# Kernel tuning notes

Hardware: AMD Instinct MI355X
Metric: run time of the kernel (lower is better)

Reference implementation:

```python
import jax, jax.numpy as jnp
import numpy as np

N_NODES, N_EDGES, NUM_GRAPHS = 50000, 800000, 64
F_DIM, H_DIM, N_LAYERS, N_CLASSES = 64, 64, 3, 16
EPS = 1e-5  # StdAggregation epsilon (PyG)


def setup_inputs() -> dict:
    key = jax.random.key(0)
    ks = jax.random.split(key, 12)
    s = 0.05
    x = jax.random.normal(ks[0], (N_NODES, F_DIM), jnp.float32)
    edge_index = jax.random.randint(ks[1], (2, N_EDGES), 0, N_NODES, dtype=jnp.int32)
    batch = jnp.sort(jax.random.randint(ks[2], (N_NODES,), 0, NUM_GRAPHS, dtype=jnp.int32))
    # per-layer PNAConv params (towers=1): pre Linear(2F->F), post Linear(13F->H), lin Linear(H->H)
    pre_w = jax.random.normal(ks[3], (N_LAYERS, F_DIM, 2 * F_DIM), jnp.float32) * s
    pre_b = jnp.zeros((N_LAYERS, F_DIM), jnp.float32)
    post_w = jax.random.normal(ks[4], (N_LAYERS, H_DIM, 13 * F_DIM), jnp.float32) * s
    post_b = jnp.zeros((N_LAYERS, H_DIM), jnp.float32)
    lin_w = jax.random.normal(ks[5], (N_LAYERS, H_DIM, H_DIM), jnp.float32) * s
    lin_b = jnp.zeros((N_LAYERS, H_DIM), jnp.float32)
    mlp_w1 = jax.random.normal(ks[6], (H_DIM, H_DIM), jnp.float32) * s
    mlp_b1 = jnp.zeros((H_DIM,), jnp.float32)
    mlp_w2 = jax.random.normal(ks[7], (N_CLASSES, H_DIM), jnp.float32) * s
    mlp_b2 = jnp.zeros((N_CLASSES,), jnp.float32)
    return dict(x=x, edge_index=edge_index, batch=batch,
                pre_w=pre_w, pre_b=pre_b, post_w=post_w, post_b=post_b,
                lin_w=lin_w, lin_b=lin_b, mlp_w1=mlp_w1, mlp_b1=mlp_b1,
                mlp_w2=mlp_w2, mlp_b2=mlp_b2)


def pna_forward(x, src, dst, pre_w, pre_b, post_w, post_b, lin_w, lin_b,
                mlp_w1, mlp_b1, mlp_w2, mlp_b2, batch):
    N = x.shape[0]
    deg_raw = jax.ops.segment_sum(jnp.ones_like(src, jnp.float32), dst, N)  # in-degree [N]
    deg = jnp.maximum(deg_raw, 1.0)[:, None]
    # avg log degree (PNA avg_deg['log'] from the degree histogram of this graph)
    avg_log = jnp.mean(jnp.log(deg_raw + 1.0))
    log_deg = jnp.log(deg + 1.0)
    amp = log_deg / avg_log          # amplification scaler [N,1]
    att = avg_log / log_deg          # attenuation scaler [N,1]
    has_in = (deg_raw > 0)[:, None]

    for l in range(pre_w.shape[0]):
        h = jnp.concatenate([x[dst], x[src]], axis=-1)        # [E, 2F] (x_i, x_j)
        m = h @ pre_w[l].T + pre_b[l]                          # pre_nn message [E, F]
        s1 = jax.ops.segment_sum(m, dst, N)
        s2 = jax.ops.segment_sum(m * m, dst, N)
        mean = s1 / deg
        std = jnp.sqrt(jax.nn.relu(s2 / deg - mean * mean) + EPS)
        mn = jnp.where(has_in, jax.ops.segment_min(m, dst, N), 0.0)
        mx = jnp.where(has_in, jax.ops.segment_max(m, dst, N), 0.0)
        aggr = jnp.concatenate([mean, mn, mx, std], axis=-1)   # [N, 4F]
        out = jnp.concatenate([x, aggr, aggr * amp, aggr * att], axis=-1)  # [N, 13F]
        out = out @ post_w[l].T + post_b[l]                    # post_nn [N, H]
        x = jax.nn.relu(out @ lin_w[l].T + lin_b[l])           # conv.lin + outer ReLU

    # global mean pool over graphs
    counts = jnp.maximum(
        jax.ops.segment_sum(jnp.ones((N,), x.dtype), batch, NUM_GRAPHS), 1.0)
    g = jax.ops.segment_sum(x, batch, NUM_GRAPHS) / counts[:, None]  # [G, H]
    g = jax.nn.relu(g @ mlp_w1.T + mlp_b1)
    return g @ mlp_w2.T + mlp_b2                               # [G, C]


def reference(x, edge_index, batch, pre_w, pre_b, post_w, post_b,
              lin_w, lin_b, mlp_w1, mlp_b1, mlp_w2, mlp_b2):
    src, dst = edge_index[0], edge_index[1]
    return pna_forward(x, src, dst, pre_w, pre_b, post_w, post_b,
                       lin_w, lin_b, mlp_w1, mlp_b1, mlp_w2, mlp_b2, batch)
```

## Files before the change

kernel.cpp:

```cpp
#include <hip/hip_runtime.h>
#include <math.h>

#define N_NODES   50000
#define N_EDGES   800000
#define NUM_GRAPHS 64
#define FDIM      64
#define HDIM      64
#define NLAYERS   3
#define NCLASSES  16
#define EPS       1e-5f

#define SCAN_CHUNK 1024
#define NCHUNKS ((N_NODES + SCAN_CHUNK - 1) / SCAN_CHUNK)

typedef unsigned short u16;
typedef unsigned int   u32;
typedef __attribute__((ext_vector_type(8))) short short8;
typedef __attribute__((ext_vector_type(4))) float floatx4;

#define WKS_LAYER 159744
#define PRES_LAYER 24576
#define KPOST_LDS_BYTES 106496

__device__ inline void split1(float f, u16& h, u16& m, u16& l) {
    u32 b  = __float_as_uint(f);
    u32 hb = b & 0xFFFF0000u;
    float r = f - __uint_as_float(hb);
    u32 mb = __float_as_uint(r) & 0xFFFF0000u;
    float r2 = r - __uint_as_float(mb);
    u32 lb = __float_as_uint(r2) & 0xFFFF0000u;
    h = (u16)(hb >> 16); m = (u16)(mb >> 16); l = (u16)(lb >> 16);
}

__device__ inline void gl_lds16(const void* g, void* l) {
    __builtin_amdgcn_global_load_lds(
        (const __attribute__((address_space(1))) u32*)g,
        (__attribute__((address_space(3))) u32*)l, 16, 0, 0);
}

__global__ __launch_bounds__(256) void k_comb(const float* __restrict__ post_w,
                                              const float* __restrict__ lin_w,
                                              const float* __restrict__ pre_w,
                                              const float* __restrict__ post_b,
                                              const float* __restrict__ lin_b,
                                              u16* __restrict__ WkS,
                                              u16* __restrict__ PreS,
                                              float* __restrict__ bcv,
                                              int* __restrict__ cnt,
                                              float* __restrict__ logsum) {
    int b = blockIdx.x, t = threadIdx.x;
    int zi = b * 256 + t;
    if (zi < N_NODES) cnt[zi] = 0;
    if (zi == 0) *logsum = 0.f;

    if (b < 624) {
        int c  = t & 63;
        int kl = t >> 6;
        int l  = b / 208;
        int o  = (b % 208) * 4 + kl;
        const float* lw = lin_w + (size_t)l * 4096 + c * 64;
        const float* pw = post_w + (size_t)l * 53248 + o;
        float acc = 0.f;
        #pragma unroll 8
        for (int j = 0; j < 64; ++j)
            acc += lw[j] * pw[(size_t)j * 832];
        u16 h, m, lo;
        split1(acc, h, m, lo);

        int kn;
        if (o < 64) kn = o;
        else {
            int s  = (o - 64) >> 8;
            int mm = (o - 64) & 255;
            int j  = mm >> 5, r = mm & 31;
            kn = 64 + j * 96 + s * 32 + r;
        }
        int ch  = kn >> 5;
        int kin = kn & 31;
        int n16 = c & 15, nt = c >> 4;
        int swk = (((kin >> 3) + (n16 >> 1)) & 3) * 8 + (kin & 7);
        size_t base = (size_t)l * WKS_LAYER + (size_t)ch * 6144
                    + nt * 512 + n16 * 32 + swk;
        WkS[base]        = h;
        WkS[base + 2048] = m;
        WkS[base + 4096] = lo;
    } else if (b == 624) {
        if (t < 192) {
            int l = t >> 6, c = t & 63;
            float acc = lin_b[l * 64 + c];
            for (int j = 0; j < 64; ++j)
                acc += lin_w[(size_t)l * 4096 + c * 64 + j] * post_b[l * 64 + j];
            bcv[l * 64 + c] = acc;
        }
    } else {
        int i = (b - 625) * 256 + t;
        int l = i >> 13;
        int rem = i & 8191;
        int c128 = rem >> 6;
        int k = rem & 63;
        float v;
        if (c128 < 64) v = pre_w[(size_t)l * 8192 + c128 * 128 + k];
        else           v = pre_w[(size_t)l * 8192 + (c128 - 64) * 128 + 64 + k];
        u16 h, m, lo;
        split1(v, h, m, lo);
        int ch = k >> 5, kin = k & 31;
        int nt = c128 >> 4, n16 = c128 & 15;
        int swk = (((kin >> 3) + (n16 >> 1)) & 3) * 8 + (kin & 7);
        size_t base = (size_t)l * PRES_LAYER + (size_t)ch * 12288
                    + nt * 512 + n16 * 32 + swk;
        PreS[base]        = h;
        PreS[base + 4096] = m;
        PreS[base + 8192] = lo;
    }
}

__global__ void k_count(const int* __restrict__ dst, int* __restrict__ cnt,
                        int* __restrict__ rank) {
    int e = blockIdx.x * 256 + threadIdx.x;
    if (e < N_EDGES) rank[e] = atomicAdd(&cnt[dst[e]], 1);
}

__global__ void k_chunk_sums(const int* __restrict__ cnt, int* __restrict__ bsum,
                             float* __restrict__ logsum) {
    __shared__ int   ired[256];
    __shared__ float lred[256];
    int b = blockIdx.x, t = threadIdx.x;
    int base = b * SCAN_CHUNK;
    int s = 0; float ls = 0.f;
    for (int i = t; i < SCAN_CHUNK; i += 256) {
        int idx = base + i;
        if (idx < N_NODES) {
            int v = cnt[idx];
            s += v;
            ls += logf((float)v + 1.0f);
        }
    }
    ired[t] = s; lred[t] = ls;
    __syncthreads();
    for (int off = 128; off > 0; off >>= 1) {
        if (t < off) { ired[t] += ired[t + off]; lred[t] += lred[t + off]; }
        __syncthreads();
    }
    if (t == 0) { bsum[b] = ired[0]; atomicAdd(logsum, lred[0]); }
}

__global__ void k_scan_top(const int* __restrict__ bsum, int* __restrict__ boff,
                           int* __restrict__ row_start) {
    if (threadIdx.x == 0) {
        int acc = 0;
        for (int i = 0; i < NCHUNKS; ++i) { boff[i] = acc; acc += bsum[i]; }
        row_start[N_NODES] = acc;
    }
}

__global__ void k_scan_chunks(const int* __restrict__ cnt, const int* __restrict__ boff,
                              int* __restrict__ row_start) {
    __shared__ int tsum[256];
    int b = blockIdx.x, t = threadIdx.x;
    int base = b * SCAN_CHUNK + t * 4;
    int v[4]; int s = 0;
    #pragma unroll
    for (int i = 0; i < 4; ++i) {
        int idx = base + i;
        v[i] = (idx < N_NODES) ? cnt[idx] : 0;
        s += v[i];
    }
    tsum[t] = s;
    __syncthreads();
    for (int off = 1; off < 256; off <<= 1) {
        int val = (t >= off) ? tsum[t - off] : 0;
        __syncthreads();
        tsum[t] += val;
        __syncthreads();
    }
    int excl = boff[b] + tsum[t] - s;
    #pragma unroll
    for (int i = 0; i < 4; ++i) {
        int idx = base + i;
        if (idx < N_NODES) row_start[idx] = excl;
        excl += v[i];
    }
}

__global__ void k_scatter(const int* __restrict__ src, const int* __restrict__ dst,
                          const int* __restrict__ rank,
                          const int* __restrict__ row_start,
                          int* __restrict__ csr_src) {
    int e = blockIdx.x * 256 + threadIdx.x;
    if (e < N_EDGES) {
        int d = dst[e];
        csr_src[row_start[d] + rank[e]] = src[e];
    }
}

__global__ void k_scal(const int* __restrict__ cnt, const float* __restrict__ logsum,
                       float* __restrict__ inv_deg, float* __restrict__ ampv,
                       float* __restrict__ attv, float* __restrict__ g_sum,
                       int* __restrict__ g_cnt) {
    int n = blockIdx.x * 256 + threadIdx.x;
    if (blockIdx.x == 0) {
        for (int i = threadIdx.x; i < 4096; i += 256) g_sum[i] = 0.f;
        if (threadIdx.x < 64) g_cnt[threadIdx.x] = 0;
    }
    if (n < N_NODES) {
        float avg = logsum[0] / (float)N_NODES;
        float degf = fmaxf((float)cnt[n], 1.0f);
        inv_deg[n] = 1.0f / degf;
        float ld = logf(degf + 1.0f);
        ampv[n] = ld / avg;
        attv[n] = avg / ld;
    }
}

__global__ __launch_bounds__(256, 4) void k_pre(const float* __restrict__ x,
                                                const u16* __restrict__ PreS,
                                                const float* __restrict__ pre_b,
                                                float* __restrict__ p,
                                                float* __restrict__ q) {
    __shared__ u16 ldsB[2 * 8192];
    int t = threadIdx.x;
    int w = t >> 6;
    int lane = t & 63;
    int m = lane & 15;
    int qh = lane >> 4;
    int rowBase = blockIdx.x * 64;

    int myrow = rowBase + 16 * w + m;
    bool vr = myrow < N_NODES;
    int crow = vr ? myrow : 0;
    const float* xrow = x + (size_t)crow * 64;

    int bo = m * 32 + ((qh + (m >> 1)) & 3) * 8;

    for (int u = w; u < 32; u += 4) {
        int ch = u >> 4, sp = (u >> 3) & 1, nt = u & 7;
        const char* g = (const char*)PreS + (size_t)ch * 24576 + sp * 8192
                      + nt * 1024 + lane * 16;
        char* l = (char*)ldsB + u * 1024;
        gl_lds16(g, l);
    }
    float fa[2][8];
    #pragma unroll
    for (int ch = 0; ch < 2; ++ch) {
        const float* sp = xrow + ch * 32 + qh * 8;
        float4 u0 = *(const float4*)sp;
        float4 u1 = *(const float4*)(sp + 4);
        fa[ch][0] = vr ? u0.x : 0.f; fa[ch][1] = vr ? u0.y : 0.f;
        fa[ch][2] = vr ? u0.z : 0.f; fa[ch][3] = vr ? u0.w : 0.f;
        fa[ch][4] = vr ? u1.x : 0.f; fa[ch][5] = vr ? u1.y : 0.f;
        fa[ch][6] = vr ? u1.z : 0.f; fa[ch][7] = vr ? u1.w : 0.f;
    }
    asm volatile("s_waitcnt vmcnt(0)" ::: "memory");
    __syncthreads();

    floatx4 acc[8] = {};
    #pragma unroll
    for (int ch = 0; ch < 2; ++ch) {
        union { u32 u[4]; short8 s8; } AH, AM;
        #pragma unroll
        for (int i = 0; i < 4; ++i) {
            float f0 = fa[ch][2 * i], f1 = fa[ch][2 * i + 1];
            u32 b0 = __float_as_uint(f0), b1 = __float_as_uint(f1);
            u32 h0 = b0 & 0xFFFF0000u,  h1 = b1 & 0xFFFF0000u;
            float r0 = f0 - __uint_as_float(h0);
            float r1 = f1 - __uint_as_float(h1);
            u32 m0 = __float_as_uint(r0) & 0xFFFF0000u;
            u32 m1 = __float_as_uint(r1) & 0xFFFF0000u;
            AH.u[i] = (h0 >> 16) | h1;
            AM.u[i] = (m0 >> 16) | m1;
        }
        const u16* Bb = ldsB + ch * 8192;
        #pragma unroll
        for (int nt = 0; nt < 8; ++nt) {
            short8 bH = *(const short8*)(Bb + nt * 512 + bo);
            short8 bM = *(const short8*)(Bb + 4096 + nt * 512 + bo);
            acc[nt] = __builtin_amdgcn_mfma_f32_16x16x32_bf16(AH.s8, bH, acc[nt], 0, 0, 0);
            acc[nt] = __builtin_amdgcn_mfma_f32_16x16x32_bf16(AH.s8, bM, acc[nt], 0, 0, 0);
            acc[nt] = __builtin_amdgcn_mfma_f32_16x16x32_bf16(AM.s8, bH, acc[nt], 0, 0, 0);
        }
    }

    int col = m;
    #pragma unroll
    for (int nt = 0; nt < 8; ++nt) {
        int cbase = (nt & 3) * 16 + col;
        float bias = (nt < 4) ? pre_b[cbase] : 0.f;
        float* outp = (nt < 4) ? p : q;
        #pragma unroll
        for (int reg = 0; reg < 4; ++reg) {
            int grow = rowBase + 16 * w + qh * 4 + reg;
            if (grow < N_NODES)
                outp[(size_t)grow * 64 + cbase] = acc[nt][reg] + bias;
        }
    }
}

__global__ __launch_bounds__(256) void k_aggr(const float* __restrict__ p,
                                              const float* __restrict__ q,
                                              const int* __restrict__ row_start,
                                              const int* __restrict__ csr_src,
                                              const float* __restrict__ inv_deg,
                                              float* __restrict__ aggr) {
    int wid  = (blockIdx.x * 256 + threadIdx.x) >> 6;
    int lane = threadIdx.x & 63;
    if (wid >= N_NODES) return;
    int n = wid;
    int beg = row_start[n], end = row_start[n + 1];
    float sum = 0.f, sq = 0.f;
    float mn = INFINITY, mx = -INFINITY;
    int e = beg;
    for (; e + 7 < end; e += 8) {
        float qv[8];
        #pragma unroll
        for (int u = 0; u < 8; ++u) {
            int s = csr_src[e + u];
            qv[u] = q[(size_t)s * 64 + lane];
        }
        #pragma unroll
        for (int u = 0; u < 8; ++u) {
            float m = qv[u];
            sum += m; sq += m * m;
            mn = fminf(mn, m); mx = fmaxf(mx, m);
        }
    }
    for (; e + 3 < end; e += 4) {
        float qv[4];
        #pragma unroll
        for (int u = 0; u < 4; ++u) {
            int s = csr_src[e + u];
            qv[u] = q[(size_t)s * 64 + lane];
        }
        #pragma unroll
        for (int u = 0; u < 4; ++u) {
            float m = qv[u];
            sum += m; sq += m * m;
            mn = fminf(mn, m); mx = fmaxf(mx, m);
        }
    }
    for (; e < end; ++e) {
        int s = csr_src[e];
        float m = q[(size_t)s * 64 + lane];
        sum += m; sq += m * m;
        mn = fminf(mn, m); mx = fmaxf(mx, m);
    }
    float* a = aggr + (size_t)n * 256;
    if (end <= beg) {
        a[lane]       = 0.f;
        a[64 + lane]  = 0.f;
        a[128 + lane] = 0.f;
        a[192 + lane] = sqrtf(EPS);
    } else {
        float pv = p[n * 64 + lane];
        float id = inv_deg[n];
        float meanq = sum * id;
        float var = fmaxf(sq * id - meanq * meanq, 0.f);
        a[lane]       = pv + meanq;
        a[64 + lane]  = pv + mn;
        a[128 + lane] = pv + mx;
        a[192 + lane] = sqrtf(var + EPS);
    }
}

__global__ __launch_bounds__(1024, 4) void k_post(const float* __restrict__ x,
                                                  const float* __restrict__ aggr,
                                                  const float* __restrict__ ampv,
                                                  const float* __restrict__ attv,
                                                  const u16* __restrict__ WkS,
                                                  const float* __restrict__ bc,
                                                  float* __restrict__ xout) {
    extern __shared__ u16 ldsB[];
    int t = threadIdx.x;
    int w = t >> 6;
    int lane = t & 63;
    int m = lane & 15;
    int qh = lane >> 4;
    int nh = blockIdx.x & 1;
    int rowBase = (blockIdx.x >> 1) * 512 + 32 * w;

    for (int u = w; u < 104; u += 16) {
        int ch = u >> 2;
        int sp = (u >> 1) & 1;
        int h2 = u & 1;
        const char* g = (const char*)WkS + ch * 12288 + sp * 4096
                      + nh * 2048 + h2 * 1024 + lane * 16;
        char* l = (char*)ldsB + u * 1024;
        gl_lds16(g, l);
    }

    int row0 = rowBase + m;
    int row1 = row0 + 16;
    int cr0 = (row0 < N_NODES) ? row0 : 0;
    int cr1 = (row1 < N_NODES) ? row1 : 0;
    const float* xr0 = x + (size_t)cr0 * 64;
    const float* xr1 = x + (size_t)cr1 * 64;
    const float* ar0 = aggr + (size_t)cr0 * 256;
    const float* ar1 = aggr + (size_t)cr1 * 256;

    int bo = m * 32 + ((qh + (m >> 1)) & 3) * 8;

    floatx4 accP0[2] = {}, accA0[2] = {}, accT0[2] = {};
    floatx4 accP1[2] = {}, accA1[2] = {}, accT1[2] = {};

    float f0[8], f1[8];
    union U8 { u32 u[4]; short8 s8; };
    U8 AH0, AM0, AH1, AM1;

    auto loadRaw = [&](const float* sp, float* f) {
        float4 u0 = *(const float4*)(sp + qh * 8);
        float4 u1 = *(const float4*)(sp + qh * 8 + 4);
        f[0] = u0.x; f[1] = u0.y; f[2] = u0.z; f[3] = u0.w;
        f[4] = u1.x; f[5] = u1.y; f[6] = u1.z; f[7] = u1.w;
    };
    auto split2 = [&](const float* f, U8& H, U8& M8) {
        #pragma unroll
        for (int i = 0; i < 4; ++i) {
            float v0 = f[2 * i], v1 = f[2 * i + 1];
            u32 b0 = __float_as_uint(v0), b1 = __float_as_uint(v1);
            u32 h0 = b0 & 0xFFFF0000u,  h1 = b1 & 0xFFFF0000u;
            float r0 = v0 - __uint_as_float(h0);
            float r1 = v1 - __uint_as_float(h1);
            u32 m0 = __float_as_uint(r0) & 0xFFFF0000u;
            u32 m1 = __float_as_uint(r1) & 0xFFFF0000u;
            H.u[i]  = (h0 >> 16) | h1;
            M8.u[i] = (m0 >> 16) | m1;
        }
    };
    #define MF(A, B, C) C = __builtin_amdgcn_mfma_f32_16x16x32_bf16((A).s8, (B), (C), 0, 0, 0)
    auto chunkMM = [&](int ch, floatx4* A0, floatx4* A1) {
        const u16* pB = ldsB + ch * 2048 + bo;
        short8 bH0 = *(const short8*)(pB);
        short8 bH1 = *(const short8*)(pB + 512);
        short8 bM0 = *(const short8*)(pB + 1024);
        short8 bM1 = *(const short8*)(pB + 1536);
        MF(AH0, bH0, A0[0]); MF(AH1, bH0, A1[0]); MF(AH0, bH1, A0[1]); MF(AH1, bH1, A1[1]);
        MF(AH0, bM0, A0[0]); MF(AH1, bM0, A1[0]); MF(AH0, bM1, A0[1]); MF(AH1, bM1, A1[1]);
        MF(AM0, bH0, A0[0]); MF(AM1, bH0, A1[0]); MF(AM0, bH1, A0[1]); MF(AM1, bH1, A1[1]);
    };

    loadRaw(xr0, f0); loadRaw(xr1, f1);
    asm volatile("s_waitcnt vmcnt(0)" ::: "memory");
    __syncthreads();

    split2(f0, AH0, AM0); split2(f1, AH1, AM1);
    loadRaw(xr0 + 32, f0); loadRaw(xr1 + 32, f1);
    chunkMM(0, accP0, accP1);
    split2(f0, AH0, AM0); split2(f1, AH1, AM1);
    loadRaw(ar0, f0); loadRaw(ar1, f1);
    chunkMM(1, accP0, accP1);
    for (int j = 0; j < 8; ++j) {
        split2(f0, AH0, AM0); split2(f1, AH1, AM1);
        if (j < 7) { loadRaw(ar0 + (j + 1) * 32, f0); loadRaw(ar1 + (j + 1) * 32, f1); }
        int ch = 2 + 3 * j;
        chunkMM(ch,     accP0, accP1);
        chunkMM(ch + 1, accA0, accA1);
        chunkMM(ch + 2, accT0, accT1);
    }
    #undef MF

    int col = m;
    #pragma unroll
    for (int frag = 0; frag < 2; ++frag) {
        #pragma unroll
        for (int reg = 0; reg < 4; ++reg) {
            int grow = rowBase + 16 * frag + qh * 4 + reg;
            if (grow < N_NODES) {
                float av = ampv[grow], tv = attv[grow];
                #pragma unroll
                for (int nt = 0; nt < 2; ++nt) {
                    int cbase = (nh * 2 + nt) * 16 + col;
                    float pv  = frag ? accP1[nt][reg] : accP0[nt][reg];
                    float av2 = frag ? accA1[nt][reg] : accA0[nt][reg];
                    float tv2 = frag ? accT1[nt][reg] : accT0[nt][reg];
                    float v = pv + av * av2 + tv * tv2 + bc[cbase];
                    xout[(size_t)grow * 64 + cbase] = fmaxf(v, 0.f);
                }
            }
        }
    }
}

__global__ __launch_bounds__(256) void k_pool(const float* __restrict__ x,
                                              const int* __restrict__ batch,
                                              float* __restrict__ g_sum,
                                              int* __restrict__ g_cnt) {
    int lane = threadIdx.x & 63;
    int wave = blockIdx.x * 4 + (threadIdx.x >> 6);
    const int NPW = 16;
    int beg = wave * NPW;
    if (beg >= N_NODES) return;
    int end = min(beg + NPW, N_NODES);
    float acc = 0.f;
    int cur = batch[beg];
    int c = 0;
    for (int n = beg; n < end; ++n) {
        int b = batch[n];
        if (b != cur) {
            atomicAdd(&g_sum[cur * 64 + lane], acc);
            if (lane == 0) atomicAdd(&g_cnt[cur], c);
            acc = 0.f; c = 0; cur = b;
        }
        acc += x[n * 64 + lane];
        ++c;
    }
    atomicAdd(&g_sum[cur * 64 + lane], acc);
    if (lane == 0) atomicAdd(&g_cnt[cur], c);
}

__global__ __launch_bounds__(256) void k_mlp(const float* __restrict__ g_sum,
                                             const int* __restrict__ g_cnt,
                                             const float* __restrict__ w1,
                                             const float* __restrict__ b1,
                                             const float* __restrict__ w2,
                                             const float* __restrict__ b2,
                                             float* __restrict__ out) {
    __shared__ float g[64][64];
    __shared__ float h[64][64];
    __shared__ float wT[64][65];
    int t = threadIdx.x;
    for (int idx = t; idx < 4096; idx += 256) {
        int gi = idx >> 6, c = idx & 63;
        float cntf = fmaxf((float)g_cnt[gi], 1.f);
        g[gi][c] = g_sum[idx] / cntf;
    }
    for (int idx = t; idx < 4096; idx += 256) {
        int c = idx >> 6, k = idx & 63;
        wT[k][c] = w1[c * 64 + k];
    }
    __syncthreads();
    for (int idx = t; idx < 4096; idx += 256) {
        int gi = idx >> 6, c = idx & 63;
        float acc = b1[c];
        for (int k = 0; k < 64; ++k) acc += g[gi][k] * wT[k][c];
        h[gi][c] = fmaxf(acc, 0.f);
    }
    __syncthreads();
    for (int idx = t; idx < 64 * NCLASSES; idx += 256) {
        int gi = idx >> 4, c = idx & 15;
        float acc = b2[c];
        for (int k = 0; k < 64; ++k) acc += h[gi][k] * w2[c * 64 + k];
        out[gi * NCLASSES + c] = acc;
    }
}

extern "C" void kernel_launch(void* const* d_in, const int* in_sizes, int n_in,
                              void* d_out, int out_size, void* d_ws, size_t ws_size,
                              hipStream_t stream) {
    const float* x      = (const float*)d_in[0];
    const int*   ei     = (const int*)d_in[1];
    const int*   batch  = (const int*)d_in[2];
    const float* pre_w  = (const float*)d_in[3];
    const float* pre_b  = (const float*)d_in[4];
    const float* post_w = (const float*)d_in[5];
    const float* post_b = (const float*)d_in[6];
    const float* lin_w  = (const float*)d_in[7];
    const float* lin_b  = (const float*)d_in[8];
    const float* mlp_w1 = (const float*)d_in[9];
    const float* mlp_b1 = (const float*)d_in[10];
    const float* mlp_w2 = (const float*)d_in[11];
    const float* mlp_b2 = (const float*)d_in[12];

    const int* src = ei;
    const int* dst = ei + N_EDGES;

    char* base = (char*)d_ws;
    size_t off = 0;
    auto alloc = [&](size_t bytes) -> void* {
        void* ptr = base + off;
        off += (bytes + 255) & ~(size_t)255;
        return ptr;
    };
    int*   cnt       = (int*)alloc(N_NODES * 4);
    int*   row_start = (int*)alloc((N_NODES + 1) * 4);
    int*   rank      = (int*)alloc(N_EDGES * 4);
    int*   csr_src   = (int*)alloc(N_EDGES * 4);
    int*   bsum      = (int*)alloc(64 * 4);
    int*   boff      = (int*)alloc(64 * 4);
    float* logsum    = (float*)alloc(16);
    float* inv_deg   = (float*)alloc(N_NODES * 4);
    float* ampv      = (float*)alloc(N_NODES * 4);
    float* attv      = (float*)alloc(N_NODES * 4);
    float* p         = (float*)alloc((size_t)N_NODES * 64 * 4);
    float* q         = (float*)alloc((size_t)N_NODES * 64 * 4);
    float* aggr      = (float*)alloc((size_t)N_NODES * 256 * 4);
    float* xb0       = (float*)alloc((size_t)N_NODES * 64 * 4);
    float* xb1       = (float*)alloc((size_t)N_NODES * 64 * 4);
    float* g_sum     = (float*)alloc(64 * 64 * 4);
    int*   g_cnt     = (int*)alloc(64 * 4);
    u16*   WkS       = (u16*)alloc((size_t)3 * WKS_LAYER * 2);
    u16*   PreS      = (u16*)alloc((size_t)3 * PRES_LAYER * 2);
    float* bcv       = (float*)alloc(3 * 64 * 4);

    k_comb<<<721, 256, 0, stream>>>(post_w, lin_w, pre_w, post_b, lin_b,
                                    WkS, PreS, bcv, cnt, logsum);

    k_count<<<(N_EDGES + 255) / 256, 256, 0, stream>>>(dst, cnt, rank);
    k_chunk_sums<<<NCHUNKS, 256, 0, stream>>>(cnt, bsum, logsum);
    k_scan_top<<<1, 64, 0, stream>>>(bsum, boff, row_start);
    k_scan_chunks<<<NCHUNKS, 256, 0, stream>>>(cnt, boff, row_start);
    k_scatter<<<(N_EDGES + 255) / 256, 256, 0, stream>>>(src, dst, rank,
                                                         row_start, csr_src);
    k_scal<<<(N_NODES + 255) / 256, 256, 0, stream>>>(cnt, logsum, inv_deg,
                                                      ampv, attv, g_sum, g_cnt);

    const int PRE_BLOCKS  = (N_NODES + 63) / 64;
    const int POST_BLOCKS = 2 * ((N_NODES + 511) / 512);
    const float* xin = x;
    float* bufs[3] = {xb0, xb1, xb0};
    for (int l = 0; l < NLAYERS; ++l) {
        k_pre<<<PRE_BLOCKS, 256, 0, stream>>>(xin, PreS + (size_t)l * PRES_LAYER,
                                              pre_b + l * 64, p, q);
        k_aggr<<<(N_NODES + 3) / 4, 256, 0, stream>>>(p, q, row_start, csr_src,
                                                      inv_deg, aggr);
        float* xo = bufs[l];
        k_post<<<POST_BLOCKS, 1024, KPOST_LDS_BYTES, stream>>>(
            xin, aggr, ampv, attv, WkS + (size_t)l * WKS_LAYER,
            bcv + l * 64, xo);
        xin = xo;
    }

    int pool_waves = (N_NODES + 15) / 16;
    k_pool<<<(pool_waves + 3) / 4, 256, 0, stream>>>(xin, batch, g_sum, g_cnt);
    k_mlp<<<1, 256, 0, stream>>>(g_sum, g_cnt, mlp_w1, mlp_b1, mlp_w2, mlp_b2,
                                 (float*)d_out);
}
```

Baseline: 415.6 us.

## Merge scan and degree-scaler kernels into one single-block kernel; remap k_post blocks

Replaces the three-kernel chunked prefix scan plus separate scaler kernel with a single 1024-thread block that computes the log-degree sum, the exclusive scan, and inv_deg/amp/att in one pass. This removes three kernel launches and their intermediate buffers. The cost is that this step now runs on one workgroup with strided per-thread loops over 49 elements each. It also remaps k_post block indices so that blocks handling the same row range are grouped in sets of 8 for locality, padding the grid to 208 blocks with an early exit.

```diff
diff --git a/kernel.cpp b/kernel.cpp
--- a/kernel.cpp
+++ b/kernel.cpp
@@ -10,9 +10,6 @@
 #define NCLASSES  16
 #define EPS       1e-5f
 
-#define SCAN_CHUNK 1024
-#define NCHUNKS ((N_NODES + SCAN_CHUNK - 1) / SCAN_CHUNK)
-
 typedef unsigned short u16;
 typedef unsigned int   u32;
 typedef __attribute__((ext_vector_type(8))) short short8;
@@ -46,12 +43,10 @@
                                               u16* __restrict__ WkS,
                                               u16* __restrict__ PreS,
                                               float* __restrict__ bcv,
-                                              int* __restrict__ cnt,
-                                              float* __restrict__ logsum) {
+                                              int* __restrict__ cnt) {
     int b = blockIdx.x, t = threadIdx.x;
     int zi = b * 256 + t;
     if (zi < N_NODES) cnt[zi] = 0;
-    if (zi == 0) *logsum = 0.f;
 
     if (b < 624) {
         int c  = t & 63;
@@ -120,66 +115,56 @@
     if (e < N_EDGES) rank[e] = atomicAdd(&cnt[dst[e]], 1);
 }
 
-__global__ void k_chunk_sums(const int* __restrict__ cnt, int* __restrict__ bsum,
-                             float* __restrict__ logsum) {
-    __shared__ int   ired[256];
-    __shared__ float lred[256];
-    int b = blockIdx.x, t = threadIdx.x;
-    int base = b * SCAN_CHUNK;
+__global__ __launch_bounds__(1024) void k_scan(const int* __restrict__ cnt,
+                                               int* __restrict__ row_start,
+                                               float* __restrict__ inv_deg,
+                                               float* __restrict__ ampv,
+                                               float* __restrict__ attv,
+                                               float* __restrict__ g_sum,
+                                               int* __restrict__ g_cnt) {
+    __shared__ int   ssum[1024];
+    __shared__ float lsum[1024];
+    __shared__ float s_avg;
+    int t = threadIdx.x;
+    const int PER = 49;
+    int beg = t * PER;
+    int end = min(beg + PER, N_NODES);
+
     int s = 0; float ls = 0.f;
-    for (int i = t; i < SCAN_CHUNK; i += 256) {
-        int idx = base + i;
-        if (idx < N_NODES) {
-            int v = cnt[idx];
-            s += v;
-            ls += logf((float)v + 1.0f);
-        }
-    }
-    ired[t] = s; lred[t] = ls;
+    for (int i = beg; i < end; ++i) {
+        int v = cnt[i];
+        s += v;
+        ls += logf((float)v + 1.0f);
+    }
+    ssum[t] = s; lsum[t] = ls;
     __syncthreads();
-    for (int off = 128; off > 0; off >>= 1) {
-        if (t < off) { ired[t] += ired[t + off]; lred[t] += lred[t + off]; }
+    for (int off = 512; off > 0; off >>= 1) {
+        if (t < off) lsum[t] += lsum[t + off];
         __syncthreads();
     }
-    if (t == 0) { bsum[b] = ired[0]; atomicAdd(logsum, lred[0]); }
-}
-
-__global__ void k_scan_top(const int* __restrict__ bsum, int* __restrict__ boff,
-                           int* __restrict__ row_start) {
-    if (threadIdx.x == 0) {
-        int acc = 0;
-        for (int i = 0; i < NCHUNKS; ++i) { boff[i] = acc; acc += bsum[i]; }
-        row_start[N_NODES] = acc;
-    }
-}
-
-__global__ void k_scan_chunks(const int* __restrict__ cnt, const int* __restrict__ boff,
-                              int* __restrict__ row_start) {
-    __shared__ int tsum[256];
-    int b = blockIdx.x, t = threadIdx.x;
-    int base = b * SCAN_CHUNK + t * 4;
-    int v[4]; int s = 0;
-    #pragma unroll
-    for (int i = 0; i < 4; ++i) {
-        int idx = base + i;
-        v[i] = (idx < N_NODES) ? cnt[idx] : 0;
-        s += v[i];
-    }
-    tsum[t] = s;
-    __syncthreads();
-    for (int off = 1; off < 256; off <<= 1) {
-        int val = (t >= off) ? tsum[t - off] : 0;
+    if (t == 0) s_avg = lsum[0] / (float)N_NODES;
+    for (int off = 1; off < 1024; off <<= 1) {
+        int v2 = (t >= off) ? ssum[t - off] : 0;
         __syncthreads();
-        tsum[t] += val;
+        ssum[t] += v2;
         __syncthreads();
     }
-    int excl = boff[b] + tsum[t] - s;
-    #pragma unroll
-    for (int i = 0; i < 4; ++i) {
-        int idx = base + i;
-        if (idx < N_NODES) row_start[idx] = excl;
-        excl += v[i];
-    }
+    float avg = s_avg;
+
+    int excl = ssum[t] - s;
+    for (int i = beg; i < end; ++i) {
+        int v = cnt[i];
+        row_start[i] = excl;
+        excl += v;
+        float degf = fmaxf((float)v, 1.0f);
+        inv_deg[i] = 1.0f / degf;
+        float ld = logf(degf + 1.0f);
+        ampv[i] = ld / avg;
+        attv[i] = avg / ld;
+    }
+    if (t == 0) row_start[N_NODES] = N_EDGES;
+    for (int i = t; i < 4096; i += 1024) g_sum[i] = 0.f;
+    if (t < 64) g_cnt[t] = 0;
 }
 
 __global__ void k_scatter(const int* __restrict__ src, const int* __restrict__ dst,
@@ -190,25 +175,6 @@
     if (e < N_EDGES) {
         int d = dst[e];
         csr_src[row_start[d] + rank[e]] = src[e];
-    }
-}
-
-__global__ void k_scal(const int* __restrict__ cnt, const float* __restrict__ logsum,
-                       float* __restrict__ inv_deg, float* __restrict__ ampv,
-                       float* __restrict__ attv, float* __restrict__ g_sum,
-                       int* __restrict__ g_cnt) {
-    int n = blockIdx.x * 256 + threadIdx.x;
-    if (blockIdx.x == 0) {
-        for (int i = threadIdx.x; i < 4096; i += 256) g_sum[i] = 0.f;
-        if (threadIdx.x < 64) g_cnt[threadIdx.x] = 0;
-    }
-    if (n < N_NODES) {
-        float avg = logsum[0] / (float)N_NODES;
-        float degf = fmaxf((float)cnt[n], 1.0f);
-        inv_deg[n] = 1.0f / degf;
-        float ld = logf(degf + 1.0f);
-        ampv[n] = ld / avg;
-        attv[n] = avg / ld;
     }
 }
 
@@ -374,17 +340,24 @@
     int lane = t & 63;
     int m = lane & 15;
     int qh = lane >> 4;
-    int nh = blockIdx.x & 1;
-    int rowBase = (blockIdx.x >> 1) * 512 + 32 * w;
+
+    int b  = blockIdx.x;
+    int s8 = b & 7;
+    int g  = b >> 3;
+    int q2 = g >> 1;
+    int nh = g & 1;
+    int r  = 8 * q2 + s8;
+    if (r >= 98) return;
+    int rowBase = r * 512 + 32 * w;
 
     for (int u = w; u < 104; u += 16) {
         int ch = u >> 2;
         int sp = (u >> 1) & 1;
         int h2 = u & 1;
-        const char* g = (const char*)WkS + ch * 12288 + sp * 4096
-                      + nh * 2048 + h2 * 1024 + lane * 16;
+        const char* gp = (const char*)WkS + ch * 12288 + sp * 4096
+                       + nh * 2048 + h2 * 1024 + lane * 16;
         char* l = (char*)ldsB + u * 1024;
-        gl_lds16(g, l);
+        gl_lds16(gp, l);
     }
 
     int row0 = rowBase + m;
@@ -402,7 +375,7 @@
     floatx4 accP1[2] = {}, accA1[2] = {}, accT1[2] = {};
 
     float f0[8], f1[8];
-    union U8 { u32 u[4]; short8 s8; };
+    union U8 { u32 u[4]; short8 s8v; };
     U8 AH0, AM0, AH1, AM1;
 
     auto loadRaw = [&](const float* sp, float* f) {
@@ -425,7 +398,7 @@
             M8.u[i] = (m0 >> 16) | m1;
         }
     };
-    #define MF(A, B, C) C = __builtin_amdgcn_mfma_f32_16x16x32_bf16((A).s8, (B), (C), 0, 0, 0)
+    #define MF(A, B, C) C = __builtin_amdgcn_mfma_f32_16x16x32_bf16((A).s8v, (B), (C), 0, 0, 0)
     auto chunkMM = [&](int ch, floatx4* A0, floatx4* A1) {
         const u16* pB = ldsB + ch * 2048 + bo;
         short8 bH0 = *(const short8*)(pB);
@@ -573,9 +546,6 @@
     int*   row_start = (int*)alloc((N_NODES + 1) * 4);
     int*   rank      = (int*)alloc(N_EDGES * 4);
     int*   csr_src   = (int*)alloc(N_EDGES * 4);
-    int*   bsum      = (int*)alloc(64 * 4);
-    int*   boff      = (int*)alloc(64 * 4);
-    float* logsum    = (float*)alloc(16);
     float* inv_deg   = (float*)alloc(N_NODES * 4);
     float* ampv      = (float*)alloc(N_NODES * 4);
     float* attv      = (float*)alloc(N_NODES * 4);
@@ -591,19 +561,16 @@
     float* bcv       = (float*)alloc(3 * 64 * 4);
 
     k_comb<<<721, 256, 0, stream>>>(post_w, lin_w, pre_w, post_b, lin_b,
-                                    WkS, PreS, bcv, cnt, logsum);
+                                    WkS, PreS, bcv, cnt);
 
     k_count<<<(N_EDGES + 255) / 256, 256, 0, stream>>>(dst, cnt, rank);
-    k_chunk_sums<<<NCHUNKS, 256, 0, stream>>>(cnt, bsum, logsum);
-    k_scan_top<<<1, 64, 0, stream>>>(bsum, boff, row_start);
-    k_scan_chunks<<<NCHUNKS, 256, 0, stream>>>(cnt, boff, row_start);
+    k_scan<<<1, 1024, 0, stream>>>(cnt, row_start, inv_deg, ampv, attv,
+                                   g_sum, g_cnt);
     k_scatter<<<(N_EDGES + 255) / 256, 256, 0, stream>>>(src, dst, rank,
                                                          row_start, csr_src);
-    k_scal<<<(N_NODES + 255) / 256, 256, 0, stream>>>(cnt, logsum, inv_deg,
-                                                      ampv, attv, g_sum, g_cnt);
 
     const int PRE_BLOCKS  = (N_NODES + 63) / 64;
-    const int POST_BLOCKS = 2 * ((N_NODES + 511) / 512);
+    const int POST_BLOCKS = 208;
     const float* xin = x;
     float* bufs[3] = {xb0, xb1, xb0};
     for (int l = 0; l < NLAYERS; ++l) {
```

New measurement: 576.2 us. +38.6%, slower.
